# Kernel optimization log

Measured on AMD Instinct MI355X. Metric: run time of the kernel, lower is better.

Reference implementation:

```python
import jax, jax.numpy as jnp
import numpy as np

# Sizes (see shape_source): N samples, D=Config.dim, H=D//2, E question types, C classes/type
N, D, H, E, C = 65536, 768, 384, 8, 8


def setup_inputs() -> dict:
    key = jax.random.key(0)
    k_x, k_t, k_w1, k_w2 = jax.random.split(key, 4)
    x = jax.random.normal(k_x, (N, D), dtype=jnp.float32)
    question_types = jax.random.randint(k_t, (N,), 0, E, dtype=jnp.int32)
    # Stacked per-type MLP head parameters (E experts)
    W1 = jax.random.normal(k_w1, (E, D, H), dtype=jnp.float32) * 0.02
    b1 = jnp.zeros((E, H), dtype=jnp.float32)
    W2 = jax.random.normal(k_w2, (E, H, C), dtype=jnp.float32) * 0.02
    b2 = jnp.zeros((E, C), dtype=jnp.float32)
    return {"x": x, "W1": W1, "b1": b1, "W2": W2, "b2": b2,
            "question_types": question_types}


def reference(x, W1, b1, W2, b2, question_types):
    # Per-sample routed 2-layer MLP head: logits_i = MLP_{type_i}(x_i).
    # Dropout is eval-mode identity. Dense-per-expert compute + mask select
    # (standard MoE reference; E is a small fixed loop, not a data-dim loop).
    n_experts = W1.shape[0]
    out = jnp.zeros((x.shape[0], W2.shape[-1]), dtype=x.dtype)
    for e in range(n_experts):
        h = jax.nn.relu(x @ W1[e] + b1[e])        # [N, H]
        logits = h @ W2[e] + b2[e]                # [N, C]
        out = jnp.where((question_types == e)[:, None], logits, out)
    return out
```

## Files before the change

kernel.cpp:

```cpp
#include <hip/hip_runtime.h>

typedef short s16x8 __attribute__((ext_vector_type(8)));
typedef float f32x4 __attribute__((ext_vector_type(4)));

#define N_SAMPLES 65536
#define DIM 768
#define HID 384
#define NEXP 8
#define NCLS 8
#define JT 24
#define KT 24

#define WS_CNT    0
#define WS_BUCKET 1024
#define WS_W1F    (WS_BUCKET + NEXP * N_SAMPLES * 4)
#define WS_XG     (WS_W1F + 8 * 576 * 64 * 8 * 2)

__device__ __forceinline__ unsigned short f2bf(float f) {
  union { float f; unsigned u; } v; v.f = f;
  unsigned r = v.u + 0x7fffu + ((v.u >> 16) & 1u);
  return (unsigned short)(r >> 16);
}

__device__ __forceinline__ unsigned cvt2(float a, float b) {
  union { float f; unsigned u; } ua, ub;
  ua.f = a; ub.f = b;
  return __builtin_amdgcn_perm(ub.u + 0x8000u, ua.u + 0x8000u, 0x07060302u);
}

#define LBAR asm volatile("s_waitcnt lgkmcnt(0)\n\ts_barrier" ::: "memory")

__global__ void k_w1frag(const float* __restrict__ W1,
                         unsigned short* __restrict__ W1F,
                         int* __restrict__ cnt) {
  if (blockIdx.x == 0 && blockIdx.y == 0 && threadIdx.x < NEXP)
    cnt[threadIdx.x] = 0;
  const int e = blockIdx.x;
  const int unit = blockIdx.y * 4 + (threadIdx.x >> 6);
  const int lane = threadIdx.x & 63;
  const int jt = unit / KT, kt = unit % KT;
  const int j = jt * 16 + (lane & 15);
  const int k0 = kt * 32 + (lane >> 4) * 8;
  const float* src = W1 + ((size_t)e * DIM + k0) * HID + j;
  s16x8 v;
#pragma unroll
  for (int i = 0; i < 8; ++i) v[i] = (short)f2bf(src[(size_t)i * HID]);
  *(s16x8*)&W1F[(((size_t)e * JT * KT + unit) * 64 + lane) * 8] = v;
}

__global__ void k_scatter(const int* __restrict__ qt, int* __restrict__ cnt,
                          int* __restrict__ bucket) {
  __shared__ int lcnt[NEXP], lbase[NEXP];
  const int t = threadIdx.x;
  const int i = blockIdx.x * 256 + t;
  if (t < NEXP) lcnt[t] = 0;
  __syncthreads();
  const int e = qt[i];
  const int rank = atomicAdd(&lcnt[e], 1);
  __syncthreads();
  if (t < NEXP) lbase[t] = atomicAdd(&cnt[t], lcnt[t]);
  __syncthreads();
  bucket[(size_t)e * N_SAMPLES + lbase[e] + rank] = i;
}

__global__ __launch_bounds__(256) void k_gather(
    const float* __restrict__ x, const int* __restrict__ cnt,
    const int* __restrict__ bucket, unsigned short* __restrict__ xg) {
  const int e = blockIdx.x;
  int base = 0, n_e = 0;
#pragma unroll
  for (int i = 0; i < NEXP; ++i) {
    int c = cnt[i];
    if (i < e) base += c;
    if (i == e) n_e = c;
  }
  const int wave = threadIdx.x >> 6, lane = threadIdx.x & 63;

  for (int rt = blockIdx.y; rt * 64 < n_e; rt += gridDim.y) {
    const int s0 = rt * 64 + wave * 16;
    int sl = s0 + (lane & 15);
    if (sl > n_e - 1) sl = n_e - 1;
    const int bkt = bucket[(size_t)e * N_SAMPLES + sl];
#pragma unroll
    for (int r = 0; r < 16; r += 2) {
      const int sA = s0 + r, sB = s0 + r + 1;
      const int srcA = __shfl(bkt, r), srcB = __shfl(bkt, r + 1);
      const float4* pa = (const float4*)(x + (size_t)srcA * DIM);
      const float4* pb = (const float4*)(x + (size_t)srcB * DIM);
      float4 c0, c1, c2, c3, c4, c5;
      if (sA < n_e) { c0 = pa[lane]; c1 = pa[64 + lane]; c2 = pa[128 + lane]; }
      if (sB < n_e) { c3 = pb[lane]; c4 = pb[64 + lane]; c5 = pb[128 + lane]; }
      if (sA < n_e) {
        uint2* da = (uint2*)(xg + (size_t)(base + sA) * DIM);
        da[lane]       = (uint2){cvt2(c0.x, c0.y), cvt2(c0.z, c0.w)};
        da[64 + lane]  = (uint2){cvt2(c1.x, c1.y), cvt2(c1.z, c1.w)};
        da[128 + lane] = (uint2){cvt2(c2.x, c2.y), cvt2(c2.z, c2.w)};
      }
      if (sB < n_e) {
        uint2* db = (uint2*)(xg + (size_t)(base + sB) * DIM);
        db[lane]       = (uint2){cvt2(c3.x, c3.y), cvt2(c3.z, c3.w)};
        db[64 + lane]  = (uint2){cvt2(c4.x, c4.y), cvt2(c4.z, c4.w)};
        db[128 + lane] = (uint2){cvt2(c5.x, c5.y), cvt2(c5.z, c5.w)};
      }
    }
  }
}


#define ALOADN(S, KS) a##S = *(const s16x8*)(ap + (KS) * 32);

#define ASTOREN(BUF, S) *(s16x8*)&(BUF)[ar * 40 + aq * 8] = a##S;

#define WLOADN(WF, KS)                                                      \
  _Pragma("unroll") for (int ni = 0; ni < 6; ++ni)                          \
      WF[ni] = *(const s16x8*)(wfbase + ((size_t)ni * KT + (KS)) * 512);

#define COMPUTE(AS, WF)                                                     \
  { _Pragma("unroll") for (int mi = 0; mi < 4; ++mi) {                      \
      s16x8 xfr = *(const s16x8*)&(AS)[(mi * 16 + lrow) * 40 + quad * 8];   \
      _Pragma("unroll") for (int ni = 0; ni < 6; ++ni)                      \
          acc[mi][ni] = __builtin_amdgcn_mfma_f32_16x16x32_bf16(            \
              WF[ni], xfr, acc[mi][ni], 0, 0, 0); } }

#define KSTEP(ASC, ASN, SN, SF, KA, WF, KW) \
  ASTOREN(ASN, SN)                          \
  ALOADN(SF, KA)                            \
  COMPUTE(ASC, WF)                          \
  WLOADN(WF, KW)                            \
  LBAR;

__global__ __launch_bounds__(256, 2) void k_moe_gemm(
    const unsigned short* __restrict__ xg, const unsigned short* __restrict__ W1F,
    const float* __restrict__ b1, const float* __restrict__ W2,
    const float* __restrict__ b2, const int* __restrict__ cnt,
    const int* __restrict__ bucket, float* __restrict__ out) {
  __shared__ __align__(16) short smem[25088];
  __shared__ __align__(16) short W2s[16 * 392];
  __shared__ float b1s[HID];
  __shared__ float b2s[NCLS];
  short* As0 = smem;
  short* As1 = smem + 2560;
  short* Hs  = smem;

  const int e = blockIdx.x;
  int base = 0, n_e = 0;
#pragma unroll
  for (int i = 0; i < NEXP; ++i) {
    int c = cnt[i];
    if (i < e) base += c;
    if (i == e) n_e = c;
  }
  if (n_e <= 0) return;
  const int t = threadIdx.x;
  const int lane = t & 63;
  const int wave = t >> 6;
  const int lrow = lane & 15;
  const int quad = lane >> 4;
  const int ar = t >> 2;
  const int aq = t & 3;

  for (int j = t; j < HID; j += 256) {
    b1s[j] = b1[e * HID + j];
    const float* wr = W2 + ((size_t)e * HID + j) * NCLS;
#pragma unroll
    for (int c = 0; c < NCLS; ++c) W2s[c * 392 + j] = (short)f2bf(wr[c]);
#pragma unroll
    for (int c = NCLS; c < 16; ++c) W2s[c * 392 + j] = 0;
  }
  if (t < NCLS) b2s[t] = b2[e * NCLS + t];

  const unsigned short* wfbase =
      W1F + ((size_t)(e * JT + wave * 6) * KT) * 512 + lane * 8;

  for (int rt = blockIdx.y; rt * 64 < n_e; rt += gridDim.y) {
    const int row0 = rt * 64;
    int rowc = row0 + ar;
    if (rowc > n_e - 1) rowc = n_e - 1;
    const unsigned short* ap = xg + (size_t)(base + rowc) * DIM + aq * 8;

    f32x4 acc[4][6];
#pragma unroll
    for (int mi = 0; mi < 4; ++mi)
#pragma unroll
      for (int ni = 0; ni < 6; ++ni) acc[mi][ni] = (f32x4){0.f, 0.f, 0.f, 0.f};

    s16x8 a0, a1, a2, a3;
    s16x8 wfA[6], wfB[6];

    ALOADN(0, 0) ALOADN(1, 1) ALOADN(2, 2) ALOADN(3, 3)
    WLOADN(wfA, 0) WLOADN(wfB, 1)
    ASTOREN(As0, 0)
    LBAR;

    for (int kb = 0; kb < 20; kb += 4) {
      KSTEP(As0, As1, 1, 0, kb + 4, wfA, kb + 2)
      KSTEP(As1, As0, 2, 1, kb + 5, wfB, kb + 3)
      KSTEP(As0, As1, 3, 2, kb + 6, wfA, kb + 4)
      KSTEP(As1, As0, 0, 3, kb + 7, wfB, kb + 5)
    }

    ASTOREN(As1, 1) COMPUTE(As0, wfA) WLOADN(wfA, 22) LBAR;
    ASTOREN(As0, 2) COMPUTE(As1, wfB) WLOADN(wfB, 23) LBAR;
    ASTOREN(As1, 3) COMPUTE(As0, wfA) LBAR;
    COMPUTE(As1, wfB) LBAR;

#pragma unroll
    for (int mi = 0; mi < 4; ++mi)
#pragma unroll
      for (int ni = 0; ni < 6; ++ni) {
        const int j = wave * 96 + ni * 16 + quad * 4;
        const float4 bb = *(const float4*)&b1s[j];
        float v0 = acc[mi][ni][0] + bb.x; v0 = v0 > 0.f ? v0 : 0.f;
        float v1 = acc[mi][ni][1] + bb.y; v1 = v1 > 0.f ? v1 : 0.f;
        float v2 = acc[mi][ni][2] + bb.z; v2 = v2 > 0.f ? v2 : 0.f;
        float v3 = acc[mi][ni][3] + bb.w; v3 = v3 > 0.f ? v3 : 0.f;
        uint2 pk = {cvt2(v0, v1), cvt2(v2, v3)};
        *(uint2*)&Hs[(mi * 16 + lrow) * 392 + j] = pk;
      }
    LBAR;

    {
      f32x4 acc2 = (f32x4){0.f, 0.f, 0.f, 0.f};
#pragma unroll
      for (int kk = 0; kk < 12; ++kk) {
        s16x8 af = *(const s16x8*)&Hs[(wave * 16 + lrow) * 392 + kk * 32 + quad * 8];
        s16x8 bf = *(const s16x8*)&W2s[lrow * 392 + kk * 32 + quad * 8];
        acc2 = __builtin_amdgcn_mfma_f32_16x16x32_bf16(af, bf, acc2, 0, 0, 0);
      }
      if (lrow < NCLS) {
        const float bb = b2s[lrow];
#pragma unroll
        for (int r = 0; r < 4; ++r) {
          const int m = wave * 16 + quad * 4 + r;
          if (row0 + m < n_e) {
            const int oi = bucket[(size_t)e * N_SAMPLES + row0 + m];
            out[(size_t)oi * NCLS + lrow] = acc2[r] + bb;
          }
        }
      }
    }
    LBAR;
  }
}

extern "C" void kernel_launch(void* const* d_in, const int* in_sizes, int n_in,
                              void* d_out, int out_size, void* d_ws, size_t ws_size,
                              hipStream_t stream) {
  const float* x  = (const float*)d_in[0];
  const float* W1 = (const float*)d_in[1];
  const float* b1 = (const float*)d_in[2];
  const float* W2 = (const float*)d_in[3];
  const float* b2 = (const float*)d_in[4];
  const int* qt   = (const int*)d_in[5];
  float* out = (float*)d_out;
  char* ws = (char*)d_ws;

  int* cnt = (int*)(ws + WS_CNT);
  int* bucket = (int*)(ws + WS_BUCKET);
  unsigned short* W1F = (unsigned short*)(ws + WS_W1F);
  unsigned short* xg  = (unsigned short*)(ws + WS_XG);

  k_w1frag<<<dim3(8, 144), dim3(256), 0, stream>>>(W1, W1F, cnt);
  k_scatter<<<dim3(256), dim3(256), 0, stream>>>(qt, cnt, bucket);
  k_gather<<<dim3(8, 128), dim3(256), 0, stream>>>(x, cnt, bucket, xg);
  k_moe_gemm<<<dim3(8, 64), dim3(256), 0, stream>>>(xg, W1F, b1, W2, b2, cnt, bucket, out);
}
```

Before: 385.4 us.

## Flatten gather over all samples and double-buffer GEMM k-steps with priority hints

The gather kernel now assigns four consecutive output rows per wave across a flat 2048-block grid. Each lane finds its expert by comparing against prefix sums, which removes the per-expert tile loop and the load imbalance between experts. The GEMM main loop now stages two k-slices of A in shared memory per barrier (four buffers instead of two), halving the number of barriers. MFMA blocks are wrapped in s_setprio raises so compute waves get issue priority over loads. This uses more LDS and adds register pressure from the extra A buffers.

```diff
diff --git a/kernel.cpp b/kernel.cpp
--- a/kernel.cpp
+++ b/kernel.cpp
@@ -29,6 +29,8 @@
 }
 
 #define LBAR asm volatile("s_waitcnt lgkmcnt(0)\n\ts_barrier" ::: "memory")
+#define SP1 __builtin_amdgcn_s_setprio(1);
+#define SP0 __builtin_amdgcn_s_setprio(0);
 
 __global__ void k_w1frag(const float* __restrict__ W1,
                          unsigned short* __restrict__ W1F,
@@ -66,43 +68,57 @@
 __global__ __launch_bounds__(256) void k_gather(
     const float* __restrict__ x, const int* __restrict__ cnt,
     const int* __restrict__ bucket, unsigned short* __restrict__ xg) {
-  const int e = blockIdx.x;
-  int base = 0, n_e = 0;
-#pragma unroll
-  for (int i = 0; i < NEXP; ++i) {
-    int c = cnt[i];
-    if (i < e) base += c;
-    if (i == e) n_e = c;
-  }
-  const int wave = threadIdx.x >> 6, lane = threadIdx.x & 63;
-
-  for (int rt = blockIdx.y; rt * 64 < n_e; rt += gridDim.y) {
-    const int s0 = rt * 64 + wave * 16;
-    int sl = s0 + (lane & 15);
-    if (sl > n_e - 1) sl = n_e - 1;
-    const int bkt = bucket[(size_t)e * N_SAMPLES + sl];
-#pragma unroll
-    for (int r = 0; r < 16; r += 2) {
-      const int sA = s0 + r, sB = s0 + r + 1;
-      const int srcA = __shfl(bkt, r), srcB = __shfl(bkt, r + 1);
-      const float4* pa = (const float4*)(x + (size_t)srcA * DIM);
-      const float4* pb = (const float4*)(x + (size_t)srcB * DIM);
-      float4 c0, c1, c2, c3, c4, c5;
-      if (sA < n_e) { c0 = pa[lane]; c1 = pa[64 + lane]; c2 = pa[128 + lane]; }
-      if (sB < n_e) { c3 = pb[lane]; c4 = pb[64 + lane]; c5 = pb[128 + lane]; }
-      if (sA < n_e) {
-        uint2* da = (uint2*)(xg + (size_t)(base + sA) * DIM);
-        da[lane]       = (uint2){cvt2(c0.x, c0.y), cvt2(c0.z, c0.w)};
-        da[64 + lane]  = (uint2){cvt2(c1.x, c1.y), cvt2(c1.z, c1.w)};
-        da[128 + lane] = (uint2){cvt2(c2.x, c2.y), cvt2(c2.z, c2.w)};
-      }
-      if (sB < n_e) {
-        uint2* db = (uint2*)(xg + (size_t)(base + sB) * DIM);
-        db[lane]       = (uint2){cvt2(c3.x, c3.y), cvt2(c3.z, c3.w)};
-        db[64 + lane]  = (uint2){cvt2(c4.x, c4.y), cvt2(c4.z, c4.w)};
-        db[128 + lane] = (uint2){cvt2(c5.x, c5.y), cvt2(c5.z, c5.w)};
-      }
+  const int lane = threadIdx.x & 63;
+  const int wid = (blockIdx.x << 2) | (threadIdx.x >> 6);
+  int b1_ = 0, b2_ = 0, b3_ = 0, b4_ = 0, b5_ = 0, b6_ = 0, b7_ = 0;
+  {
+    int a = cnt[0];
+    b1_ = a; a += cnt[1]; b2_ = a; a += cnt[2]; b3_ = a; a += cnt[3];
+    b4_ = a; a += cnt[4]; b5_ = a; a += cnt[5]; b6_ = a; a += cnt[6];
+    b7_ = a;
+  }
+#pragma unroll
+  for (int it = 0; it < 2; ++it) {
+    const int s0 = (wid + it * 8192) * 4;
+    int src = 0;
+    if (lane < 4) {
+      const int sl = s0 + lane;
+      int e = 0, bs = 0;
+      if (sl >= b1_) { e = 1; bs = b1_; }
+      if (sl >= b2_) { e = 2; bs = b2_; }
+      if (sl >= b3_) { e = 3; bs = b3_; }
+      if (sl >= b4_) { e = 4; bs = b4_; }
+      if (sl >= b5_) { e = 5; bs = b5_; }
+      if (sl >= b6_) { e = 6; bs = b6_; }
+      if (sl >= b7_) { e = 7; bs = b7_; }
+      src = bucket[(size_t)e * N_SAMPLES + (sl - bs)];
     }
+    const int r0 = __shfl(src, 0), r1 = __shfl(src, 1),
+              r2 = __shfl(src, 2), r3 = __shfl(src, 3);
+    const float4* p0 = (const float4*)(x + (size_t)r0 * DIM);
+    const float4* p1 = (const float4*)(x + (size_t)r1 * DIM);
+    const float4* p2 = (const float4*)(x + (size_t)r2 * DIM);
+    const float4* p3 = (const float4*)(x + (size_t)r3 * DIM);
+    float4 c00 = p0[lane], c01 = p0[64 + lane], c02 = p0[128 + lane];
+    float4 c10 = p1[lane], c11 = p1[64 + lane], c12 = p1[128 + lane];
+    float4 c20 = p2[lane], c21 = p2[64 + lane], c22 = p2[128 + lane];
+    float4 c30 = p3[lane], c31 = p3[64 + lane], c32 = p3[128 + lane];
+    uint2* d0 = (uint2*)(xg + (size_t)(s0 + 0) * DIM);
+    uint2* d1 = (uint2*)(xg + (size_t)(s0 + 1) * DIM);
+    uint2* d2 = (uint2*)(xg + (size_t)(s0 + 2) * DIM);
+    uint2* d3 = (uint2*)(xg + (size_t)(s0 + 3) * DIM);
+    d0[lane]       = (uint2){cvt2(c00.x, c00.y), cvt2(c00.z, c00.w)};
+    d0[64 + lane]  = (uint2){cvt2(c01.x, c01.y), cvt2(c01.z, c01.w)};
+    d0[128 + lane] = (uint2){cvt2(c02.x, c02.y), cvt2(c02.z, c02.w)};
+    d1[lane]       = (uint2){cvt2(c10.x, c10.y), cvt2(c10.z, c10.w)};
+    d1[64 + lane]  = (uint2){cvt2(c11.x, c11.y), cvt2(c11.z, c11.w)};
+    d1[128 + lane] = (uint2){cvt2(c12.x, c12.y), cvt2(c12.z, c12.w)};
+    d2[lane]       = (uint2){cvt2(c20.x, c20.y), cvt2(c20.z, c20.w)};
+    d2[64 + lane]  = (uint2){cvt2(c21.x, c21.y), cvt2(c21.z, c21.w)};
+    d2[128 + lane] = (uint2){cvt2(c22.x, c22.y), cvt2(c22.z, c22.w)};
+    d3[lane]       = (uint2){cvt2(c30.x, c30.y), cvt2(c30.z, c30.w)};
+    d3[64 + lane]  = (uint2){cvt2(c31.x, c31.y), cvt2(c31.z, c31.w)};
+    d3[128 + lane] = (uint2){cvt2(c32.x, c32.y), cvt2(c32.z, c32.w)};
   }
 }
 
@@ -121,13 +137,6 @@
       _Pragma("unroll") for (int ni = 0; ni < 6; ++ni)                      \
           acc[mi][ni] = __builtin_amdgcn_mfma_f32_16x16x32_bf16(            \
               WF[ni], xfr, acc[mi][ni], 0, 0, 0); } }
-
-#define KSTEP(ASC, ASN, SN, SF, KA, WF, KW) \
-  ASTOREN(ASN, SN)                          \
-  ALOADN(SF, KA)                            \
-  COMPUTE(ASC, WF)                          \
-  WLOADN(WF, KW)                            \
-  LBAR;
 
 __global__ __launch_bounds__(256, 2) void k_moe_gemm(
     const unsigned short* __restrict__ xg, const unsigned short* __restrict__ W1F,
@@ -140,6 +149,8 @@
   __shared__ float b2s[NCLS];
   short* As0 = smem;
   short* As1 = smem + 2560;
+  short* As2 = smem + 5120;
+  short* As3 = smem + 7680;
   short* Hs  = smem;
 
   const int e = blockIdx.x;
@@ -189,20 +200,28 @@
 
     ALOADN(0, 0) ALOADN(1, 1) ALOADN(2, 2) ALOADN(3, 3)
     WLOADN(wfA, 0) WLOADN(wfB, 1)
-    ASTOREN(As0, 0)
+    ASTOREN(As0, 0) ASTOREN(As1, 1)
     LBAR;
 
     for (int kb = 0; kb < 20; kb += 4) {
-      KSTEP(As0, As1, 1, 0, kb + 4, wfA, kb + 2)
-      KSTEP(As1, As0, 2, 1, kb + 5, wfB, kb + 3)
-      KSTEP(As0, As1, 3, 2, kb + 6, wfA, kb + 4)
-      KSTEP(As1, As0, 0, 3, kb + 7, wfB, kb + 5)
+      ASTOREN(As2, 2) ASTOREN(As3, 3)
+      ALOADN(0, kb + 4) ALOADN(1, kb + 5)
+      SP1 COMPUTE(As0, wfA) SP0 WLOADN(wfA, kb + 2)
+      SP1 COMPUTE(As1, wfB) SP0 WLOADN(wfB, kb + 3)
+      LBAR;
+      ASTOREN(As0, 0) ASTOREN(As1, 1)
+      ALOADN(2, kb + 6) ALOADN(3, kb + 7)
+      SP1 COMPUTE(As2, wfA) SP0 WLOADN(wfA, kb + 4)
+      SP1 COMPUTE(As3, wfB) SP0 WLOADN(wfB, kb + 5)
+      LBAR;
     }
-
-    ASTOREN(As1, 1) COMPUTE(As0, wfA) WLOADN(wfA, 22) LBAR;
-    ASTOREN(As0, 2) COMPUTE(As1, wfB) WLOADN(wfB, 23) LBAR;
-    ASTOREN(As1, 3) COMPUTE(As0, wfA) LBAR;
-    COMPUTE(As1, wfB) LBAR;
+    ASTOREN(As2, 2) ASTOREN(As3, 3)
+    SP1 COMPUTE(As0, wfA) SP0 WLOADN(wfA, 22)
+    SP1 COMPUTE(As1, wfB) SP0 WLOADN(wfB, 23)
+    LBAR;
+    SP1 COMPUTE(As2, wfA) SP0
+    SP1 COMPUTE(As3, wfB) SP0
+    LBAR;
 
 #pragma unroll
     for (int mi = 0; mi < 4; ++mi)
@@ -262,6 +281,6 @@
 
   k_w1frag<<<dim3(8, 144), dim3(256), 0, stream>>>(W1, W1F, cnt);
   k_scatter<<<dim3(256), dim3(256), 0, stream>>>(qt, cnt, bucket);
-  k_gather<<<dim3(8, 128), dim3(256), 0, stream>>>(x, cnt, bucket, xg);
+  k_gather<<<dim3(2048), dim3(256), 0, stream>>>(x, cnt, bucket, xg);
   k_moe_gemm<<<dim3(8, 64), dim3(256), 0, stream>>>(xg, W1F, b1, W2, b2, cnt, bucket, out);
 }
```

Result: no change. 383.7 us (-0.4%).
